# Optimization experiments

Measured on AMD Instinct MI355X. Metric: run time of the kernel, lower is better.

## Reference

```python
import jax, jax.numpy as jnp
import numpy as np

H = 8  # num_heads in both MHA blocks


def _mha_self(x, W_in, b_in, W_out, b_out, mask=None):
    """Faithful nn.MultiheadAttention self-attention (batch_first).
    x: [B,S,E]; W_in: [3E,E]; b_in: [3E]; W_out: [E,E]; b_out: [E].
    mask: optional [S,S] bool, True = attend."""
    B, S, E = x.shape
    dh = E // H
    qkv = x @ W_in.T + b_in                      # [B,S,3E]
    q, k, v = jnp.split(qkv, 3, axis=-1)
    # [B,H,S,dh]
    q = q.reshape(B, S, H, dh).transpose(0, 2, 1, 3)
    k = k.reshape(B, S, H, dh).transpose(0, 2, 1, 3)
    v = v.reshape(B, S, H, dh).transpose(0, 2, 1, 3)
    scores = jnp.einsum('bhqd,bhkd->bhqk', q, k) / jnp.sqrt(jnp.asarray(dh, x.dtype))
    if mask is not None:
        scores = jnp.where(mask[None, None], scores, jnp.finfo(scores.dtype).min)
    probs = jax.nn.softmax(scores, axis=-1)
    out = jnp.einsum('bhqk,bhkd->bhqd', probs, v)  # [B,H,S,dh]
    out = out.transpose(0, 2, 1, 3).reshape(B, S, E)
    return out @ W_out.T + b_out


def setup_inputs() -> dict:
    key = jax.random.key(0)
    ks = jax.random.split(key, 7)
    B, S, E = 8, 1024, 512
    sc = 0.02
    return {
        'x': jax.random.normal(ks[0], (B, S, E), jnp.float32),
        'Wl_in': jax.random.normal(ks[1], (3 * E, E), jnp.float32) * sc,
        'bl_in': jnp.zeros((3 * E,), jnp.float32),
        'Wl_out': jax.random.normal(ks[2], (E, E), jnp.float32) * sc,
        'bl_out': jnp.zeros((E,), jnp.float32),
        'Wg_in': jax.random.normal(ks[3], (3 * E, E), jnp.float32) * sc,
        'bg_in': jnp.zeros((3 * E,), jnp.float32),
        'Wg_out': jax.random.normal(ks[4], (E, E), jnp.float32) * sc,
        'bg_out': jnp.zeros((E,), jnp.float32),
        'Wf': jax.random.normal(ks[5], (E, 2 * E), jnp.float32) * sc,
        'bf': jnp.zeros((E,), jnp.float32),
    }


def reference(x, Wl_in, bl_in, Wl_out, bl_out, Wg_in, bg_in, Wg_out, bg_out, Wf, bf):
    LOCAL = 3  # local_size
    B, S, E = x.shape
    # Per-token sliding window [i-LOCAL, i+LOCAL] == banded attention mask
    idx = jnp.arange(S)
    band = jnp.abs(idx[:, None] - idx[None, :]) <= LOCAL  # [S,S] bool
    local_out = _mha_self(x, Wl_in, bl_in, Wl_out, bl_out, mask=band)
    global_out = _mha_self(x, Wg_in, bg_in, Wg_out, bg_out)
    fused = jnp.concatenate([local_out, global_out], axis=-1)  # [B,S,2E]
    return jax.nn.relu(fused @ Wf.T + bf)
```

## Files before the change

kernel.cpp:

```cpp
#include <hip/hip_runtime.h>

typedef unsigned short u16;
typedef unsigned int   u32;
typedef __bf16 v8bf __attribute__((ext_vector_type(8)));
typedef float  v4f  __attribute__((ext_vector_type(4)));
typedef u16    us4  __attribute__((ext_vector_type(4)));
typedef u32    ui4  __attribute__((ext_vector_type(4)));

__device__ __forceinline__ u16 f2bf(float f) {
  u32 u = __builtin_bit_cast(u32, f);
  u += 0x7fffu + ((u >> 16) & 1u);
  return (u16)(u >> 16);
}
__device__ __forceinline__ float bf2f(u16 s) {
  u32 u = ((u32)s) << 16;
  return __builtin_bit_cast(float, u);
}

__device__ __forceinline__ void load_lds16(const u16* g, u16* l) {
  __builtin_amdgcn_global_load_lds(
      (const __attribute__((address_space(1))) u32*)g,
      (__attribute__((address_space(3))) u32*)l, 16, 0, 0);
}

__global__ void __launch_bounds__(256) cvt_all(
    const float* __restrict__ x,   const float* __restrict__ wli,
    const float* __restrict__ wlo, const float* __restrict__ wgi,
    const float* __restrict__ wgo, const float* __restrict__ wf,
    u16* __restrict__ out, u16* __restrict__ wloT, u16* __restrict__ wgoT)
{
  const int v = blockIdx.x * 256 + threadIdx.x;
  const float* src; int obase; int mode = 0; u16* T = nullptr;
  if      (v < 1048576) { src = x;   obase = 0;       }
  else if (v < 1245184) { src = wli; obase = 1048576; }
  else if (v < 1310720) { src = wlo; obase = 1245184; mode = 1; T = wloT; }
  else if (v < 1507328) { src = wgi; obase = 1310720; }
  else if (v < 1572864) { src = wgo; obase = 1507328; mode = 1; T = wgoT; }
  else                  { src = wf;  obase = 1572864; }
  const int rel = v - obase;
  const float4 f = reinterpret_cast<const float4*>(src)[rel];
  us4 o;
  o.x = f2bf(f.x); o.y = f2bf(f.y); o.z = f2bf(f.z); o.w = f2bf(f.w);
  if (mode) {
    const int eb = rel * 4, c = eb >> 9, k = eb & 511;
#pragma unroll
    for (int i = 0; i < 4; ++i) T[(k + i) * 512 + c] = o[i];
  } else {
    int o4;
    if      (v < 1245184) o4 = v;
    else if (v < 1507328) o4 = v - 65536;
    else                  o4 = v - 131072;
    reinterpret_cast<us4*>(out)[o4] = o;
  }
}

template<int RELU, int OUTF32, int TV, int BIASF>
__device__ __forceinline__ void gemm_body(
    u16* __restrict__ As, u16* __restrict__ Bs,
    const u16* __restrict__ A, const int lda,
    const u16* __restrict__ B, const int ldb,
    const float* __restrict__ bias, void* __restrict__ C,
    u16* __restrict__ vt, const int bm, const int bn,
    const int K, const int ldc, const int colofs)
{
  const int tid  = threadIdx.x;
  const int lane = tid & 63;
  const int w    = tid >> 6;
  const int lid  = lane & 15;
  const int quad = lane >> 4;
  const int wr = w >> 1, wc = w & 1;

  v4f acc[4][4];
#pragma unroll
  for (int i = 0; i < 4; ++i)
#pragma unroll
    for (int j = 0; j < 4; ++j)
      acc[i][j] = (v4f){0.f, 0.f, 0.f, 0.f};

  const int dr = lane >> 3;
  const int cs = ((lane ^ dr) & 7) * 8;

  for (int k0 = 0; k0 < K; k0 += 64) {
#pragma unroll
    for (int p = 0; p < 4; ++p) {
      const int g   = w + p * 4;
      const int row = g * 8 + dr;
      load_lds16(A + (size_t)(bm + row) * lda + k0 + cs, As + g * 512);
      load_lds16(B + (size_t)(bn + row) * ldb + k0 + cs, Bs + g * 512);
    }
    __syncthreads();
#pragma unroll
    for (int kk = 0; kk < 2; ++kk) {
      v8bf af[4], bfr[4];
#pragma unroll
      for (int mi = 0; mi < 4; ++mi)
        af[mi] = *reinterpret_cast<const v8bf*>(
            &As[(wr * 64 + mi * 16 + lid) * 64 + (((kk * 4 + quad) ^ (lid & 7)) * 8)]);
#pragma unroll
      for (int ni = 0; ni < 4; ++ni)
        bfr[ni] = *reinterpret_cast<const v8bf*>(
            &Bs[(wc * 64 + ni * 16 + lid) * 64 + (((kk * 4 + quad) ^ (lid & 7)) * 8)]);
#pragma unroll
      for (int mi = 0; mi < 4; ++mi)
#pragma unroll
        for (int ni = 0; ni < 4; ++ni)
          acc[mi][ni] = __builtin_amdgcn_mfma_f32_16x16x32_bf16(
              af[mi], bfr[ni], acc[mi][ni], 0, 0, 0);
    }
    __syncthreads();
  }

  float bv[4];
#pragma unroll
  for (int ni = 0; ni < 4; ++ni)
    bv[ni] = BIASF ? bias[bn + wc * 64 + ni * 16 + lid] : 0.f;

  if (TV && bn >= 1024) {
#pragma unroll
    for (int mi = 0; mi < 4; ++mi) {
      const int m0 = bm + wr * 64 + mi * 16 + quad * 4;
#pragma unroll
      for (int ni = 0; ni < 4; ++ni) {
        const int n = bn + wc * 64 + ni * 16 + lid - 1024;
        us4 pk;
#pragma unroll
        for (int r = 0; r < 4; ++r) pk[r] = f2bf(acc[mi][ni][r] + bv[ni]);
        const size_t idx =
            ((size_t)((m0 >> 10) * 8 + (n >> 6)) * 64 + (n & 63)) * 1024 + (m0 & 1023);
        *reinterpret_cast<us4*>(&vt[idx]) = pk;
      }
    }
  } else {
#pragma unroll
    for (int mi = 0; mi < 4; ++mi) {
#pragma unroll
      for (int ni = 0; ni < 4; ++ni) {
        const int n = bn + wc * 64 + ni * 16 + lid;
#pragma unroll
        for (int r = 0; r < 4; ++r) {
          const int m = bm + wr * 64 + mi * 16 + quad * 4 + r;
          float v = acc[mi][ni][r] + bv[ni];
          if (RELU) v = fmaxf(v, 0.f);
          if (OUTF32)
            reinterpret_cast<float*>(C)[(size_t)m * ldc + colofs + n] = v;
          else
            reinterpret_cast<u16*>(C)[(size_t)m * ldc + colofs + n] = f2bf(v);
        }
      }
    }
  }
}

__global__ void __launch_bounds__(256) qkv_dual(
    const u16* __restrict__ xb,
    const u16* __restrict__ wli, const float* __restrict__ bli, u16* __restrict__ qkv_l,
    const u16* __restrict__ wgi, const float* __restrict__ bgi, u16* __restrict__ qkv_g,
    u16* __restrict__ vt)
{
  __shared__ __align__(16) u16 As[128 * 64];
  __shared__ __align__(16) u16 Bs[128 * 64];
  if (blockIdx.x < 12)
    gemm_body<0,0,0,1>(As, Bs, xb, 512, wli, 512, bli, qkv_l, nullptr,
                       blockIdx.y * 128, blockIdx.x * 128, 512, 1536, 0);
  else
    gemm_body<0,0,1,1>(As, Bs, xb, 512, wgi, 512, bgi, qkv_g, vt,
                       blockIdx.y * 128, (blockIdx.x - 12) * 128, 512, 1536, 0);
}

__global__ void __launch_bounds__(256, 4) mega(
    const u16* __restrict__ qkv, const u16* __restrict__ vt, u16* __restrict__ outp,
    const u16* __restrict__ wfb, const u16* __restrict__ wloT, const u16* __restrict__ wgoT,
    u16* __restrict__ Wc, const float* __restrict__ blo, const float* __restrict__ bgo,
    const float* __restrict__ bff, float* __restrict__ bias_c,
    const u16* __restrict__ qkvl, u16* __restrict__ attn_l)
{
  __shared__ __align__(16) u16 smem[20480];
  const int bx   = blockIdx.x;
  const int tid  = threadIdx.x;
  const int lane = tid & 63;
  const int w    = tid >> 6;

  if (bx >= 1064) {
    const int lbx = bx - 1064;
    const int qt = lbx & 15, bh = lbx >> 4;
    const int b = bh >> 3, h = bh & 7;
    const int i0 = qt * 64;
    const size_t base = (size_t)b * 1024 * 1536;
    u16* Kl = smem;
    u16* Vl = smem + 5040;

    for (int i2 = tid; i2 < 1120; i2 += 256) {
      const int isV = i2 >= 560;
      const int i3  = isV ? i2 - 560 : i2;
      const int row = i3 >> 3, ch = i3 & 7;
      const int jc = min(max(i0 - 3 + row, 0), 1023);
      const ui4 d = *reinterpret_cast<const ui4*>(
          qkvl + base + (size_t)jc * 1536 + (isV ? 1024 : 512) + h * 64 + ch * 8);
      *reinterpret_cast<ui4*>(&(isV ? Vl : Kl)[row * 72 + ch * 8]) = d;
    }
    __syncthreads();

    const int q   = lane >> 2;
    const int oct = lane & 3;
    const int i   = i0 + w * 16 + q;
    const u16* qrow = qkvl + base + (size_t)i * 1536 + h * 64 + oct * 16;
    float qf[16];
    {
      const v8bf q0 = *reinterpret_cast<const v8bf*>(qrow);
      const v8bf q1 = *reinterpret_cast<const v8bf*>(qrow + 8);
#pragma unroll
      for (int e = 0; e < 8; ++e) { qf[e] = (float)q0[e]; qf[8 + e] = (float)q1[e]; }
    }
    float denom = 0.f, accv[16];
#pragma unroll
    for (int e = 0; e < 16; ++e) accv[e] = 0.f;

#pragma unroll
    for (int tt = 0; tt < 7; ++tt) {
      const int j = i - 3 + tt;
      const bool ok = (j >= 0) && (j <= 1023);
      const int ridx = w * 16 + q + tt;
      const v8bf k0 = *reinterpret_cast<const v8bf*>(&Kl[ridx * 72 + oct * 16]);
      const v8bf k1 = *reinterpret_cast<const v8bf*>(&Kl[ridx * 72 + oct * 16 + 8]);
      float pr = 0.f;
#pragma unroll
      for (int e = 0; e < 8; ++e)
        pr += qf[e] * (float)k0[e] + qf[8 + e] * (float)k1[e];
      pr += __shfl_xor(pr, 1);
      pr += __shfl_xor(pr, 2);
      const float p = ok ? __expf(pr * 0.125f) : 0.f;
      denom += p;
      const v8bf v0 = *reinterpret_cast<const v8bf*>(&Vl[ridx * 72 + oct * 16]);
      const v8bf v1 = *reinterpret_cast<const v8bf*>(&Vl[ridx * 72 + oct * 16 + 8]);
#pragma unroll
      for (int e = 0; e < 8; ++e) {
        accv[e]     += p * (float)v0[e];
        accv[8 + e] += p * (float)v1[e];
      }
    }
    const float inv = 1.f / denom;
    u16* dst = attn_l + (size_t)(b * 1024 + i) * 1536 + h * 64 + oct * 16;
#pragma unroll
    for (int c4 = 0; c4 < 4; ++c4) {
      us4 pk;
#pragma unroll
      for (int e = 0; e < 4; ++e) pk[e] = f2bf(accv[c4 * 4 + e] * inv);
      *reinterpret_cast<us4*>(dst + c4 * 4) = pk;
    }
    return;
  }
  if (bx >= 1056) {
    const int e = (bx - 1056) * 64 + w * 16;
    for (int t = 0; t < 16; ++t) {
      float sum = 0.f;
#pragma unroll
      for (int j = 0; j < 16; ++j) {
        const int c2 = j * 64 + lane;
        const float b = (c2 < 512) ? blo[c2] : bgo[c2 - 512];
        sum += bf2f(wfb[(size_t)(e + t) * 1024 + c2]) * b;
      }
#pragma unroll
      for (int msk = 32; msk >= 1; msk >>= 1) sum += __shfl_xor(sum, msk);
      if (lane == 0) bias_c[e + t] = bff[e + t] + sum;
    }
    return;
  }
  if (bx >= 1024) {
    const int idx = bx - 1024;
    const int half = idx >> 4, rem = idx & 15;
    gemm_body<0,0,0,0>(smem, smem + 8192, wfb + half * 512, 1024,
                       (half ? wgoT : wloT), 512, nullptr, Wc, nullptr,
                       (rem >> 2) * 128, (rem & 3) * 128, 512, 1024, half * 512);
    return;
  }

  const int lid  = lane & 15;
  const int quad = lane >> 4;
  const int qt = (bx >> 3) & 15;
  const int bh = ((bx & 7) << 3) | (bx >> 7);
  const int b = bh >> 3, h = bh & 7;
  const size_t base = (size_t)b * 1024 * 1536;

  v8bf aq[2];
  {
    const size_t qoff = base + (size_t)(qt * 64 + w * 16 + lid) * 1536 + h * 64 + quad * 8;
    aq[0] = *reinterpret_cast<const v8bf*>(qkv + qoff);
    aq[1] = *reinterpret_cast<const v8bf*>(qkv + qoff + 32);
#pragma unroll
    for (int k = 0; k < 2; ++k)
#pragma unroll
      for (int i = 0; i < 8; ++i)
        aq[k][i] = (__bf16)((float)aq[k][i] * 0.125f);
  }
  v8bf ones;
#pragma unroll
  for (int i = 0; i < 8; ++i) ones[i] = (__bf16)1.0f;

  v4f o[4], lacc = (v4f){0.f, 0.f, 0.f, 0.f};
#pragma unroll
  for (int nd = 0; nd < 4; ++nd) o[nd] = (v4f){0.f, 0.f, 0.f, 0.f};

  u16* Ps = smem + 16384;
  const int dr = lane >> 3;
  const int dc = lane & 7;
#define STAGE(KT, BI)                                                          \
  {                                                                            \
    _Pragma("unroll") for (int p = 0; p < 2; ++p) {                            \
      const int r = (w + p * 4) * 8 + dr;                                      \
      const int cs = (dc ^ (r & 7)) * 8;                                       \
      load_lds16(qkv + base + (size_t)((KT) * 64 + r) * 1536 + 512 + h * 64 + cs, \
                 smem + (BI) * 4096 + (w + p * 4) * 512);                      \
      load_lds16(vt + ((size_t)bh * 64 + r) * 1024 + (KT) * 64 + cs,           \
                 smem + 8192 + (BI) * 4096 + (w + p * 4) * 512);               \
    }                                                                          \
  }
  STAGE(0, 0);

  for (int kt = 0; kt < 16; ++kt) {
    __syncthreads();
    if (kt < 15) STAGE(kt + 1, (kt + 1) & 1);
    const u16* Ks = smem + (kt & 1) * 4096;
    const u16* Vs = smem + 8192 + (kt & 1) * 4096;

    v4f s[4];
#pragma unroll
    for (int nk = 0; nk < 4; ++nk) s[nk] = (v4f){0.f, 0.f, 0.f, 0.f};
#pragma unroll
    for (int kk = 0; kk < 2; ++kk)
#pragma unroll
      for (int nk = 0; nk < 4; ++nk) {
        const v8bf bk = *reinterpret_cast<const v8bf*>(
            &Ks[(nk * 16 + lid) * 64 + (((kk * 4 + quad) ^ (lid & 7)) * 8)]);
        s[nk] = __builtin_amdgcn_mfma_f32_16x16x32_bf16(aq[kk], bk, s[nk], 0, 0, 0);
      }

#pragma unroll
    for (int nk = 0; nk < 4; ++nk) {
#pragma unroll
      for (int r = 0; r < 4; ++r) {
        const float p = __expf(s[nk][r]);
        const int prow = quad * 4 + r;
        const int pcol = nk * 16 + lid;
        Ps[w * 1024 + prow * 64 + (((pcol >> 3) ^ (prow & 7)) * 8) + (pcol & 7)] =
            (u16)(__builtin_bit_cast(u32, p) >> 16);
      }
    }

#pragma unroll
    for (int kk = 0; kk < 2; ++kk) {
      const v8bf ap = *reinterpret_cast<const v8bf*>(
          &Ps[w * 1024 + lid * 64 + (((kk * 4 + quad) ^ (lid & 7)) * 8)]);
      lacc = __builtin_amdgcn_mfma_f32_16x16x32_bf16(ones, ap, lacc, 0, 0, 0);
#pragma unroll
      for (int nd = 0; nd < 4; ++nd) {
        const v8bf av = *reinterpret_cast<const v8bf*>(
            &Vs[(nd * 16 + lid) * 64 + (((kk * 4 + quad) ^ (lid & 7)) * 8)]);
        o[nd] = __builtin_amdgcn_mfma_f32_16x16x32_bf16(av, ap, o[nd], 0, 0, 0);
      }
    }
  }
#undef STAGE

  const float inv = 1.f / lacc[0];
  const int tok = b * 1024 + qt * 64 + w * 16 + lid;
#pragma unroll
  for (int nd = 0; nd < 4; ++nd) {
    us4 pk;
#pragma unroll
    for (int r = 0; r < 4; ++r) pk[r] = f2bf(o[nd][r] * inv);
    *reinterpret_cast<us4*>(&outp[(size_t)tok * 512 + h * 64 + nd * 16 + quad * 4]) = pk;
  }
}

__global__ void __launch_bounds__(256) gemm_final(
    const u16* __restrict__ Al, const u16* __restrict__ Ag,
    const u16* __restrict__ Bw, const float* __restrict__ biasc,
    float* __restrict__ out)
{
  __shared__ __align__(16) u16 As[64 * 64];
  __shared__ __align__(16) u16 Bs[128 * 64];
  const int tid  = threadIdx.x;
  const int lane = tid & 63;
  const int w    = tid >> 6;
  const int lid  = lane & 15;
  const int quad = lane >> 4;
  const int bm = blockIdx.y * 64;
  const int bn = blockIdx.x * 128;

  v4f acc[4][2];
#pragma unroll
  for (int i = 0; i < 4; ++i)
#pragma unroll
    for (int j = 0; j < 2; ++j)
      acc[i][j] = (v4f){0.f, 0.f, 0.f, 0.f};

  const int dr = lane >> 3;
  const int cs = ((lane ^ dr) & 7) * 8;

  for (int k0 = 0; k0 < 1024; k0 += 64) {
    const int half = k0 >> 9;
    const u16* Asrc = half ? Ag : Al;
    const int  lda  = half ? 512 : 1536;
    const int  kcol = k0 & 511;
#pragma unroll
    for (int p = 0; p < 2; ++p) {
      const int g   = w + p * 4;
      const int row = g * 8 + dr;
      load_lds16(Asrc + (size_t)(bm + row) * lda + kcol + cs, As + g * 512);
    }
#pragma unroll
    for (int p = 0; p < 4; ++p) {
      const int g   = w + p * 4;
      const int row = g * 8 + dr;
      load_lds16(Bw + (size_t)(bn + row) * 1024 + k0 + cs, Bs + g * 512);
    }
    __syncthreads();
#pragma unroll
    for (int kk = 0; kk < 2; ++kk) {
      v8bf af[4], bfr[2];
#pragma unroll
      for (int mi = 0; mi < 4; ++mi)
        af[mi] = *reinterpret_cast<const v8bf*>(
            &As[(mi * 16 + lid) * 64 + (((kk * 4 + quad) ^ (lid & 7)) * 8)]);
#pragma unroll
      for (int ni = 0; ni < 2; ++ni)
        bfr[ni] = *reinterpret_cast<const v8bf*>(
            &Bs[(w * 32 + ni * 16 + lid) * 64 + (((kk * 4 + quad) ^ (lid & 7)) * 8)]);
#pragma unroll
      for (int mi = 0; mi < 4; ++mi)
#pragma unroll
        for (int ni = 0; ni < 2; ++ni)
          acc[mi][ni] = __builtin_amdgcn_mfma_f32_16x16x32_bf16(
              af[mi], bfr[ni], acc[mi][ni], 0, 0, 0);
    }
    __syncthreads();
  }

#pragma unroll
  for (int mi = 0; mi < 4; ++mi) {
#pragma unroll
    for (int ni = 0; ni < 2; ++ni) {
      const int n = bn + w * 32 + ni * 16 + lid;
      const float bv = biasc[n];
#pragma unroll
      for (int r = 0; r < 4; ++r) {
        const int m = bm + mi * 16 + quad * 4 + r;
        out[(size_t)m * 512 + n] = fmaxf(acc[mi][ni][r] + bv, 0.f);
      }
    }
  }
}

extern "C" void kernel_launch(void* const* d_in, const int* in_sizes, int n_in,
                              void* d_out, int out_size, void* d_ws, size_t ws_size,
                              hipStream_t stream) {
  (void)in_sizes; (void)n_in; (void)out_size; (void)ws_size;
  const float* x   = (const float*)d_in[0];
  const float* Wli = (const float*)d_in[1];
  const float* bli = (const float*)d_in[2];
  const float* Wlo = (const float*)d_in[3];
  const float* blo = (const float*)d_in[4];
  const float* Wgi = (const float*)d_in[5];
  const float* bgi = (const float*)d_in[6];
  const float* Wgo = (const float*)d_in[7];
  const float* bgo = (const float*)d_in[8];
  const float* Wf  = (const float*)d_in[9];
  const float* bff = (const float*)d_in[10];
  float* out = (float*)d_out;

  u16* W      = (u16*)d_ws;
  u16* xb     = W + 0;
  u16* wli    = W + 4194304;
  u16* wgi    = W + 4980736;
  u16* wfb    = W + 5767168;
  u16* qkv_l  = W + 6291456;
  u16* qkv_g  = W + 18874368;
  u16* vt     = W + 31457280;
  u16* Wc     = W + 35651584;
  float* bias_c = (float*)(W + 36175872);
  u16* wloT   = W + 36176896;
  u16* wgoT   = W + 36439040;
  u16* attn_g = W + 0;
  u16* attn_l = qkv_g + 1024;

  cvt_all<<<6656, 256, 0, stream>>>(x, Wli, Wlo, Wgi, Wgo, Wf, W, wloT, wgoT);
  qkv_dual<<<dim3(24, 64), 256, 0, stream>>>(xb, wli, bli, qkv_l, wgi, bgi, qkv_g, vt);
  mega<<<2088, 256, 0, stream>>>(qkv_g, vt, attn_g, wfb, wloT, wgoT, Wc,
                                 blo, bgo, bff, bias_c, qkv_l, attn_l);
  gemm_final<<<dim3(4, 128), 256, 0, stream>>>(attn_l, attn_g, Wc, bias_c, out);
}
```

Baseline: 182.6 us.

## Double query rows per attention block to reuse K/V tiles across two subtiles

The global-attention part of the fused kernel now handles 128 query rows per block instead of 64. Each wave processes two 16-row subtiles and shares the K and V fragments it loads from LDS between them, which halves K/V global-to-LDS traffic per query and halves the number of attention blocks. LDS grows for the larger P buffer, and occupancy is lowered from 4 to 3 blocks per CU. The fused kernel has fewer blocks, which may reduce parallelism and leave tail imbalance against the local-attention and weight-fusion blocks.

Measured after the change: 180.6 us. About the same (-1.1%).

```diff
diff --git a/kernel.cpp b/kernel.cpp
--- a/kernel.cpp
+++ b/kernel.cpp
@@ -167,21 +167,21 @@
                        blockIdx.y * 128, (blockIdx.x - 12) * 128, 512, 1536, 0);
 }
 
-__global__ void __launch_bounds__(256, 4) mega(
+__global__ void __launch_bounds__(256, 3) mega(
     const u16* __restrict__ qkv, const u16* __restrict__ vt, u16* __restrict__ outp,
     const u16* __restrict__ wfb, const u16* __restrict__ wloT, const u16* __restrict__ wgoT,
     u16* __restrict__ Wc, const float* __restrict__ blo, const float* __restrict__ bgo,
     const float* __restrict__ bff, float* __restrict__ bias_c,
     const u16* __restrict__ qkvl, u16* __restrict__ attn_l)
 {
-  __shared__ __align__(16) u16 smem[20480];
+  __shared__ __align__(16) u16 smem[24576];
   const int bx   = blockIdx.x;
   const int tid  = threadIdx.x;
   const int lane = tid & 63;
   const int w    = tid >> 6;
 
-  if (bx >= 1064) {
-    const int lbx = bx - 1064;
+  if (bx >= 552) {
+    const int lbx = bx - 552;
     const int qt = lbx & 15, bh = lbx >> 4;
     const int b = bh >> 3, h = bh & 7;
     const int i0 = qt * 64;
@@ -249,8 +249,8 @@
     }
     return;
   }
-  if (bx >= 1056) {
-    const int e = (bx - 1056) * 64 + w * 16;
+  if (bx >= 544) {
+    const int e = (bx - 544) * 64 + w * 16;
     for (int t = 0; t < 16; ++t) {
       float sum = 0.f;
 #pragma unroll
@@ -265,8 +265,8 @@
     }
     return;
   }
-  if (bx >= 1024) {
-    const int idx = bx - 1024;
+  if (bx >= 512) {
+    const int idx = bx - 512;
     const int half = idx >> 4, rem = idx & 15;
     gemm_body<0,0,0,0>(smem, smem + 8192, wfb + half * 512, 1024,
                        (half ? wgoT : wloT), 512, nullptr, Wc, nullptr,
@@ -276,29 +276,35 @@
 
   const int lid  = lane & 15;
   const int quad = lane >> 4;
-  const int qt = (bx >> 3) & 15;
-  const int bh = ((bx & 7) << 3) | (bx >> 7);
+  const int qt = (bx >> 3) & 7;
+  const int bh = ((bx & 7) << 3) | (bx >> 6);
   const int b = bh >> 3, h = bh & 7;
   const size_t base = (size_t)b * 1024 * 1536;
 
-  v8bf aq[2];
-  {
-    const size_t qoff = base + (size_t)(qt * 64 + w * 16 + lid) * 1536 + h * 64 + quad * 8;
-    aq[0] = *reinterpret_cast<const v8bf*>(qkv + qoff);
-    aq[1] = *reinterpret_cast<const v8bf*>(qkv + qoff + 32);
+  v8bf aq[2][2];
+#pragma unroll
+  for (int qs = 0; qs < 2; ++qs) {
+    const size_t qoff =
+        base + (size_t)(qt * 128 + w * 32 + qs * 16 + lid) * 1536 + h * 64 + quad * 8;
+    aq[qs][0] = *reinterpret_cast<const v8bf*>(qkv + qoff);
+    aq[qs][1] = *reinterpret_cast<const v8bf*>(qkv + qoff + 32);
 #pragma unroll
     for (int k = 0; k < 2; ++k)
 #pragma unroll
       for (int i = 0; i < 8; ++i)
-        aq[k][i] = (__bf16)((float)aq[k][i] * 0.125f);
+        aq[qs][k][i] = (__bf16)((float)aq[qs][k][i] * 0.125f);
   }
   v8bf ones;
 #pragma unroll
   for (int i = 0; i < 8; ++i) ones[i] = (__bf16)1.0f;
 
-  v4f o[4], lacc = (v4f){0.f, 0.f, 0.f, 0.f};
-#pragma unroll
-  for (int nd = 0; nd < 4; ++nd) o[nd] = (v4f){0.f, 0.f, 0.f, 0.f};
+  v4f o[2][4], lacc[2];
+#pragma unroll
+  for (int qs = 0; qs < 2; ++qs) {
+    lacc[qs] = (v4f){0.f, 0.f, 0.f, 0.f};
+#pragma unroll
+    for (int nd = 0; nd < 4; ++nd) o[qs][nd] = (v4f){0.f, 0.f, 0.f, 0.f};
+  }
 
   u16* Ps = smem + 16384;
   const int dr = lane >> 3;
@@ -322,53 +328,72 @@
     const u16* Ks = smem + (kt & 1) * 4096;
     const u16* Vs = smem + 8192 + (kt & 1) * 4096;
 
-    v4f s[4];
-#pragma unroll
-    for (int nk = 0; nk < 4; ++nk) s[nk] = (v4f){0.f, 0.f, 0.f, 0.f};
+    v8bf bk[2][4];
 #pragma unroll
     for (int kk = 0; kk < 2; ++kk)
 #pragma unroll
+      for (int nk = 0; nk < 4; ++nk)
+        bk[kk][nk] = *reinterpret_cast<const v8bf*>(
+            &Ks[(nk * 16 + lid) * 64 + (((kk * 4 + quad) ^ (lid & 7)) * 8)]);
+
+#pragma unroll
+    for (int qs = 0; qs < 2; ++qs) {
+      v4f s[4];
+#pragma unroll
+      for (int nk = 0; nk < 4; ++nk) s[nk] = (v4f){0.f, 0.f, 0.f, 0.f};
+#pragma unroll
+      for (int kk = 0; kk < 2; ++kk)
+#pragma unroll
+        for (int nk = 0; nk < 4; ++nk)
+          s[nk] = __builtin_amdgcn_mfma_f32_16x16x32_bf16(
+              aq[qs][kk], bk[kk][nk], s[nk], 0, 0, 0);
+#pragma unroll
       for (int nk = 0; nk < 4; ++nk) {
-        const v8bf bk = *reinterpret_cast<const v8bf*>(
-            &Ks[(nk * 16 + lid) * 64 + (((kk * 4 + quad) ^ (lid & 7)) * 8)]);
-        s[nk] = __builtin_amdgcn_mfma_f32_16x16x32_bf16(aq[kk], bk, s[nk], 0, 0, 0);
-      }
-
-#pragma unroll
-    for (int nk = 0; nk < 4; ++nk) {
-#pragma unroll
-      for (int r = 0; r < 4; ++r) {
-        const float p = __expf(s[nk][r]);
-        const int prow = quad * 4 + r;
-        const int pcol = nk * 16 + lid;
-        Ps[w * 1024 + prow * 64 + (((pcol >> 3) ^ (prow & 7)) * 8) + (pcol & 7)] =
-            (u16)(__builtin_bit_cast(u32, p) >> 16);
+#pragma unroll
+        for (int r = 0; r < 4; ++r) {
+          const float p = __expf(s[nk][r]);
+          const int prow = quad * 4 + r;
+          const int pcol = nk * 16 + lid;
+          Ps[w * 2048 + qs * 1024 + prow * 64 +
+             (((pcol >> 3) ^ (prow & 7)) * 8) + (pcol & 7)] =
+              (u16)(__builtin_bit_cast(u32, p) >> 16);
+        }
       }
     }
 
 #pragma unroll
     for (int kk = 0; kk < 2; ++kk) {
-      const v8bf ap = *reinterpret_cast<const v8bf*>(
-          &Ps[w * 1024 + lid * 64 + (((kk * 4 + quad) ^ (lid & 7)) * 8)]);
-      lacc = __builtin_amdgcn_mfma_f32_16x16x32_bf16(ones, ap, lacc, 0, 0, 0);
-#pragma unroll
-      for (int nd = 0; nd < 4; ++nd) {
-        const v8bf av = *reinterpret_cast<const v8bf*>(
+      v8bf av[4];
+#pragma unroll
+      for (int nd = 0; nd < 4; ++nd)
+        av[nd] = *reinterpret_cast<const v8bf*>(
             &Vs[(nd * 16 + lid) * 64 + (((kk * 4 + quad) ^ (lid & 7)) * 8)]);
-        o[nd] = __builtin_amdgcn_mfma_f32_16x16x32_bf16(av, ap, o[nd], 0, 0, 0);
+#pragma unroll
+      for (int qs = 0; qs < 2; ++qs) {
+        const v8bf ap = *reinterpret_cast<const v8bf*>(
+            &Ps[w * 2048 + qs * 1024 + lid * 64 + (((kk * 4 + quad) ^ (lid & 7)) * 8)]);
+        lacc[qs] = __builtin_amdgcn_mfma_f32_16x16x32_bf16(ones, ap, lacc[qs], 0, 0, 0);
+#pragma unroll
+        for (int nd = 0; nd < 4; ++nd)
+          o[qs][nd] = __builtin_amdgcn_mfma_f32_16x16x32_bf16(
+              av[nd], ap, o[qs][nd], 0, 0, 0);
       }
     }
   }
 #undef STAGE
 
-  const float inv = 1.f / lacc[0];
-  const int tok = b * 1024 + qt * 64 + w * 16 + lid;
-#pragma unroll
-  for (int nd = 0; nd < 4; ++nd) {
-    us4 pk;
-#pragma unroll
-    for (int r = 0; r < 4; ++r) pk[r] = f2bf(o[nd][r] * inv);
-    *reinterpret_cast<us4*>(&outp[(size_t)tok * 512 + h * 64 + nd * 16 + quad * 4]) = pk;
+#pragma unroll
+  for (int qs = 0; qs < 2; ++qs) {
+    const float inv = 1.f / lacc[qs][0];
+    const int tok = b * 1024 + qt * 128 + w * 32 + qs * 16 + lid;
+#pragma unroll
+    for (int nd = 0; nd < 4; ++nd) {
+      us4 pk;
+#pragma unroll
+      for (int r = 0; r < 4; ++r) pk[r] = f2bf(o[qs][nd][r] * inv);
+      *reinterpret_cast<us4*>(
+          &outp[(size_t)tok * 512 + h * 64 + nd * 16 + quad * 4]) = pk;
+    }
   }
 }
 
@@ -485,7 +510,7 @@
 
   cvt_all<<<6656, 256, 0, stream>>>(x, Wli, Wlo, Wgi, Wgo, Wf, W, wloT, wgoT);
   qkv_dual<<<dim3(24, 64), 256, 0, stream>>>(xb, wli, bli, qkv_l, wgi, bgi, qkv_g, vt);
-  mega<<<2088, 256, 0, stream>>>(qkv_g, vt, attn_g, wfb, wloT, wgoT, Wc,
+  mega<<<1576, 256, 0, stream>>>(qkv_g, vt, attn_g, wfb, wloT, wgoT, Wc,
                                  blo, bgo, bff, bias_c, qkv_l, attn_l);
   gemm_final<<<dim3(4, 128), 256, 0, stream>>>(attn_l, attn_g, Wc, bias_c, out);
 }
```
